# Optimization experiments

Measured on AMD Instinct MI355X. Metric: run time of the kernel, lower is better.

The kernel has to match this reference:

```python
import jax, jax.numpy as jnp
import numpy as np
from jax import lax

T = 512
CHUNK = 64
H = W = 28
C = 4
D_MODEL = H * W * C  # 3136
D_HIDDEN = 512
ALPHA = 0.9
ETA0 = 0.1
P = 2.0
EPS = 1e-6


def setup_inputs() -> dict:
    key = jax.random.key(0)
    ks = jax.random.split(key, 8)
    x = jax.random.normal(ks[0], (T, C, H, W), dtype=jnp.float32)
    conv_k_w = jax.random.normal(ks[1], (3, 3, C, C), dtype=jnp.float32) / 6.0  # lecun-ish: fan_in=36
    conv_v_w = jax.random.normal(ks[2], (3, 3, C, C), dtype=jnp.float32) / 6.0
    conv_k_b = jnp.zeros((C,), jnp.float32)
    conv_v_b = jnp.zeros((C,), jnp.float32)
    rms_k_scale = jnp.ones((C,), jnp.float32)
    rms_v_scale = jnp.ones((C,), jnp.float32)
    W1 = jax.random.normal(ks[3], (D_MODEL, D_HIDDEN), dtype=jnp.float32) / np.sqrt(D_MODEL).astype(np.float32)
    b1 = jnp.zeros((D_HIDDEN,), jnp.float32)
    W2 = jax.random.normal(ks[4], (D_HIDDEN, D_MODEL), dtype=jnp.float32) / np.sqrt(D_HIDDEN).astype(np.float32)
    b2 = jnp.zeros((D_MODEL,), jnp.float32)
    return {"x": x, "conv_k_w": conv_k_w, "conv_k_b": conv_k_b,
            "conv_v_w": conv_v_w, "conv_v_b": conv_v_b,
            "rms_k_scale": rms_k_scale, "rms_v_scale": rms_v_scale,
            "W1": W1, "b1": b1, "W2": W2, "b2": b2}


def _conv(x_nhwc, w, b):
    y = lax.conv_general_dilated(x_nhwc, w, window_strides=(1, 1), padding='SAME',
                                 dimension_numbers=('NHWC', 'HWIO', 'NHWC'))
    return y + b


def _rmsnorm(z, scale):
    inv = lax.rsqrt(jnp.mean(z * z, axis=-1, keepdims=True) + EPS)
    return z * inv * scale


def _mlp(params, k):
    w1, bb1, w2, bb2 = params
    return jax.nn.gelu(k @ w1 + bb1) @ w2 + bb2


def reference(x, conv_k_w, conv_k_b, conv_v_w, conv_v_b, rms_k_scale, rms_v_scale, W1, b1, W2, b2):
    t = x.shape[0]
    xh = jnp.transpose(x, (0, 2, 3, 1))  # [T,H,W,C]
    nk = _rmsnorm(_conv(xh, conv_k_w, conv_k_b), rms_k_scale).reshape(t, -1)  # [T, D_MODEL]
    nv = _rmsnorm(_conv(xh, conv_v_w, conv_v_b), rms_v_scale).reshape(t, -1)

    params0 = (W1, b1, W2, b2)

    def loss_per_token(params, k, v):
        pred = _mlp(params, k)
        return jnp.sum(jnp.abs(pred - v) ** P)

    etas = ETA0 * ALPHA ** jnp.arange(CHUNK, dtype=jnp.float32)
    betas = ALPHA ** jnp.arange(CHUNK, dtype=jnp.float32)
    weights = etas * (betas[-1] / betas)  # [CHUNK]

    n_chunks = t // CHUNK
    Kc = nk.reshape(n_chunks, CHUNK, D_MODEL)
    Vc = nv.reshape(n_chunks, CHUNK, D_MODEL)

    def chunk_body(params, kv):
        K, V = kv
        # per-token parameter grads: leaves have leading CHUNK axis
        grads = jax.vmap(jax.grad(loss_per_token), in_axes=(None, 0, 0))(params, K, V)
        new_params = jax.tree.map(
            lambda p, g: p - jnp.tensordot(weights, g, axes=((0,), (0,))), params, grads)
        Y = _mlp(new_params, K)  # recall on keys with updated fast weights
        return new_params, Y

    _, Y_chunks = lax.scan(chunk_body, params0, (Kc, Vc))
    Y = Y_chunks.reshape(t, D_MODEL)
    return Y.reshape(t, C, H, W)
```

## Files before the change

### kernel.cpp

```cpp
#include <hip/hip_runtime.h>
#include <math.h>

#define DM 3136
#define DH 512

typedef __attribute__((ext_vector_type(8))) short bf16x8;
typedef __attribute__((ext_vector_type(4))) float f32x4;

__device__ __forceinline__ ushort f2bf(float f) {
  union { float f; unsigned u; } v; v.f = f;
  unsigned r = v.u + 0x7FFFu + ((v.u >> 16) & 1u);
  return (ushort)(r >> 16);
}
__device__ __forceinline__ float bf2f(ushort u) {
  union { float f; unsigned u; } v; v.u = ((unsigned)u) << 16;
  return v.f;
}

#define MICRO_4x4 \
    acc[0][0] += a.x*b.x; acc[0][1] += a.x*b.y; acc[0][2] += a.x*b.z; acc[0][3] += a.x*b.w; \
    acc[1][0] += a.y*b.x; acc[1][1] += a.y*b.y; acc[1][2] += a.y*b.z; acc[1][3] += a.y*b.w; \
    acc[2][0] += a.z*b.x; acc[2][1] += a.z*b.y; acc[2][2] += a.z*b.z; acc[2][3] += a.z*b.w; \
    acc[3][0] += a.w*b.x; acc[3][1] += a.w*b.y; acc[3][2] += a.w*b.z; acc[3][3] += a.w*b.w;

__device__ __forceinline__ void gelu_both(float xx, float& g, float& gp) {
  const float c = 0.7978845608028654f;
  const float a = 0.044715f;
  float x2 = xx * xx;
  float u = c * (xx + a * xx * x2);
  float t = tanhf(u);
  g  = 0.5f * xx * (1.f + t);
  gp = 0.5f * (1.f + t) + 0.5f * xx * (1.f - t * t) * c * (1.f + 3.f * a * x2);
}
__device__ __forceinline__ float gelu_only(float xx) {
  const float c = 0.7978845608028654f;
  const float a = 0.044715f;
  float u = c * (xx + a * xx * xx * xx);
  return 0.5f * xx * (1.f + tanhf(u));
}

__device__ __forceinline__ void nt64_core(
    const ushort* __restrict__ A, int lda,
    const ushort* __restrict__ B, int ldb,
    int ksteps, f32x4* acc) {
  int lane = threadIdx.x & 63;
  int wv = threadIdx.x >> 6;
  int qr = wv >> 1, qc = wv & 1;
  int lr = lane & 15;
  int lk = (lane >> 4) << 3;
  const ushort* pa0 = A + (size_t)(qr * 32 + lr) * lda + lk;
  const ushort* pa1 = pa0 + (size_t)16 * lda;
  const ushort* pb0 = B + (size_t)(qc * 32 + lr) * ldb + lk;
  const ushort* pb1 = pb0 + (size_t)16 * ldb;
  bf16x8 a0 = *(const bf16x8*)pa0;
  bf16x8 a1 = *(const bf16x8*)pa1;
  bf16x8 b0 = *(const bf16x8*)pb0;
  bf16x8 b1 = *(const bf16x8*)pb1;
  for (int s = 0; s < ksteps; ++s) {
    int sn = (s + 1 < ksteps) ? (s + 1) * 32 : s * 32;
    bf16x8 na0 = *(const bf16x8*)(pa0 + sn);
    bf16x8 na1 = *(const bf16x8*)(pa1 + sn);
    bf16x8 nb0 = *(const bf16x8*)(pb0 + sn);
    bf16x8 nb1 = *(const bf16x8*)(pb1 + sn);
    acc[0] = __builtin_amdgcn_mfma_f32_16x16x32_bf16(a0, b0, acc[0], 0, 0, 0);
    acc[1] = __builtin_amdgcn_mfma_f32_16x16x32_bf16(a0, b1, acc[1], 0, 0, 0);
    acc[2] = __builtin_amdgcn_mfma_f32_16x16x32_bf16(a1, b0, acc[2], 0, 0, 0);
    acc[3] = __builtin_amdgcn_mfma_f32_16x16x32_bf16(a1, b1, acc[3], 0, 0, 0);
    a0 = na0; a1 = na1; b0 = nb0; b1 = nb1;
  }
}

__device__ __forceinline__ void nt64_store(const f32x4* acc, float* __restrict__ dst, int ldc) {
  int lane = threadIdx.x & 63, wv = threadIdx.x >> 6;
  int r0 = (wv >> 1) * 32 + ((lane >> 4) << 2);
  int c0 = (wv & 1) * 32 + (lane & 15);
  #pragma unroll
  for (int r = 0; r < 4; ++r) {
    dst[(size_t)(r0 + r) * ldc + c0]           = acc[0][r];
    dst[(size_t)(r0 + r) * ldc + c0 + 16]      = acc[1][r];
    dst[(size_t)(r0 + r + 16) * ldc + c0]      = acc[2][r];
    dst[(size_t)(r0 + r + 16) * ldc + c0 + 16] = acc[3][r];
  }
}

__device__ __forceinline__ void dw_epilogue256(
    const f32x4* acc, int n0, const float* __restrict__ Vn,
    const float* __restrict__ b2in, float wc2,
    ushort* __restrict__ Dwb_o, ushort* __restrict__ Dwt_o,
    float* __restrict__ b2out, float* smem) {
  int lane = threadIdx.x & 63, wvv = threadIdx.x >> 6;
  int qr = wvv >> 1, qc = wvv & 1;
  int r0 = qr * 32 + ((lane >> 4) << 2);
  int c0 = qc * 32 + (lane & 15);
  float csum[2] = {0.f, 0.f};
  #pragma unroll
  for (int r = 0; r < 4; ++r) {
    #pragma unroll
    for (int p = 0; p < 4; ++p) {
      int m = r0 + r + ((p >> 1) ? 16 : 0);
      int dl = c0 + ((p & 1) ? 16 : 0);
      int d = n0 + dl;
      float dw = wc2 * (acc[p][r] + b2in[d] - Vn[(size_t)m * DM + d]);
      ushort db = f2bf(dw);
      Dwb_o[(size_t)m * DM + d] = db;
      Dwt_o[(size_t)d * 64 + m] = db;
      csum[p & 1] += dw;
    }
  }
  int slot = qr * 4 + ((lane >> 4) & 3);
  smem[(size_t)c0 * 8 + slot] = csum[0];
  smem[(size_t)(c0 + 16) * 8 + slot] = csum[1];
  __syncthreads();
  if (threadIdx.x < 64) {
    float s = 0.f;
    #pragma unroll
    for (int q = 0; q < 8; ++q) s += smem[threadIdx.x * 8 + q];
    b2out[n0 + threadIdx.x] = b2in[n0 + threadIdx.x] - s;
  }
}

__global__ __launch_bounds__(256) void conv_rms(
    const float* __restrict__ x,
    const float* __restrict__ wk, const float* __restrict__ bk,
    const float* __restrict__ wv, const float* __restrict__ bv,
    const float* __restrict__ sk, const float* __restrict__ sv,
    const float* __restrict__ W1, ushort* __restrict__ w1tb,
    const float* __restrict__ W2, ushort* __restrict__ W2b0, ushort* __restrict__ W2tb0,
    ushort* __restrict__ nkb, float* __restrict__ nv) {
  __shared__ float smem[4160];
  int tid = threadIdx.x;
  if (blockIdx.x >= 1960) {
    int t = blockIdx.x - 1960;
    int d0 = (t % 49) * 64, h0 = (t / 49) * 64;
    int c = tid & 63, rq = tid >> 6;
    #pragma unroll
    for (int q = 0; q < 16; ++q) {
      int r = q * 4 + rq;
      float v = W2[(size_t)(h0 + r) * DM + d0 + c];
      smem[r * 65 + c] = v;
      W2b0[(size_t)(h0 + r) * DM + d0 + c] = f2bf(v);
    }
    __syncthreads();
    #pragma unroll
    for (int q = 0; q < 16; ++q) {
      int r = q * 4 + rq;
      W2tb0[(size_t)(d0 + r) * DH + h0 + c] = f2bf(smem[c * 65 + r]);
    }
    return;
  }
  if (blockIdx.x >= 1568) {
    int t = blockIdx.x - 1568;
    int d0 = (t % 49) * 64, h0 = (t / 49) * 64;
    int c = tid & 63, rq = tid >> 6;
    #pragma unroll
    for (int q = 0; q < 16; ++q) {
      int r = q * 4 + rq;
      smem[r * 65 + c] = W1[(size_t)(d0 + r) * 512 + h0 + c];
    }
    __syncthreads();
    #pragma unroll
    for (int q = 0; q < 16; ++q) {
      int r = q * 4 + rq;
      w1tb[(size_t)(h0 + r) * 3136 + d0 + c] = f2bf(smem[c * 65 + r]);
    }
    return;
  }
  float* swk = smem;
  float* swv = smem + 144;
  float* sb  = smem + 288;
  if (tid < 144) { swk[tid] = wk[tid]; swv[tid] = wv[tid]; }
  if (tid < 4) {
    sb[tid] = bk[tid]; sb[4 + tid] = bv[tid];
    sb[8 + tid] = sk[tid]; sb[12 + tid] = sv[tid];
  }
  __syncthreads();
  int idx = blockIdx.x * 256 + tid;
  int t = idx / 784, hw = idx - t * 784;
  int h = hw / 28, w = hw - h * 28;
  float ak[4], av[4];
  #pragma unroll
  for (int c = 0; c < 4; ++c) { ak[c] = sb[c]; av[c] = sb[4 + c]; }
  const float* xt = x + (size_t)t * DM;
  for (int kh = 0; kh < 3; ++kh) {
    int ih = h + kh - 1;
    if (ih < 0 || ih >= 28) continue;
    for (int kw = 0; kw < 3; ++kw) {
      int iw = w + kw - 1;
      if (iw < 0 || iw >= 28) continue;
      int base = (kh * 3 + kw) * 16;
      #pragma unroll
      for (int ci = 0; ci < 4; ++ci) {
        float xv = xt[ci * 784 + ih * 28 + iw];
        #pragma unroll
        for (int co = 0; co < 4; ++co) {
          ak[co] += xv * swk[base + ci * 4 + co];
          av[co] += xv * swv[base + ci * 4 + co];
        }
      }
    }
  }
  float mk = (ak[0]*ak[0] + ak[1]*ak[1] + ak[2]*ak[2] + ak[3]*ak[3]) * 0.25f + 1e-6f;
  float mv = (av[0]*av[0] + av[1]*av[1] + av[2]*av[2] + av[3]*av[3]) * 0.25f + 1e-6f;
  float ik = 1.f / sqrtf(mk), iv = 1.f / sqrtf(mv);
  ushort4 ok = { f2bf(ak[0]*ik*sb[8]), f2bf(ak[1]*ik*sb[9]),
                 f2bf(ak[2]*ik*sb[10]), f2bf(ak[3]*ik*sb[11]) };
  float4 ov = { av[0]*iv*sb[12], av[1]*iv*sb[13], av[2]*iv*sb[14], av[3]*iv*sb[15] };
  *(ushort4*)&nkb[(size_t)idx * 4] = ok;
  *(float4*)&nv[(size_t)idx * 4] = ov;
}

__global__ __launch_bounds__(256) void u1_kernel(
    const ushort* __restrict__ nkb, const ushort* __restrict__ w1tb,
    float* __restrict__ KKsl, float* __restrict__ Hb_sl) {
  f32x4 acc[4] = {{0.f,0.f,0.f,0.f},{0.f,0.f,0.f,0.f},{0.f,0.f,0.f,0.f},{0.f,0.f,0.f,0.f}};
  int job = blockIdx.x;
  if (job < 448) {
    int s = job % 7;
    int t = job / 7;
    int m0 = (t >> 3) * 64, n0 = (t & 7) * 64;
    nt64_core(nkb + (size_t)m0 * DM + s * 448, DM, w1tb + (size_t)n0 * DM + s * 448, DM, 14, acc);
    nt64_store(acc, Hb_sl + (size_t)s * 262144 + (size_t)m0 * 512 + n0, 512);
  } else {
    int j2 = job - 448;
    int p = j2 / 7, s = j2 % 7;
    int c = 0;
    while ((c + 1) * (c + 2) / 2 <= p) ++c;
    int j = p - c * (c + 1) / 2;
    nt64_core(nkb + (size_t)c * 64 * DM + s * 448, DM, nkb + (size_t)j * 64 * DM + s * 448, DM, 14, acc);
    nt64_store(acc, KKsl + ((size_t)p * 7 + s) * 4096, 64);
  }
}

__global__ __launch_bounds__(256) void u2_kernel(
    const float* __restrict__ KKsl, const float* __restrict__ Hb_sl,
    float* __restrict__ KKf, float* __restrict__ Hbase,
    const float* __restrict__ b1,
    float* __restrict__ Hh, ushort* __restrict__ Gb, ushort* __restrict__ Gtb,
    float* __restrict__ Gp) {
  int i = blockIdx.x * 256 + threadIdx.x;
  if (i < 147456) {
    int pair = i >> 12, e = i & 4095;
    float s = 0.f;
    #pragma unroll
    for (int t = 0; t < 7; ++t) s += KKsl[((size_t)pair * 7 + t) * 4096 + e];
    KKf[i] = s;
  } else {
    int j = i - 147456;
    float s = 0.f;
    #pragma unroll
    for (int t = 0; t < 7; ++t) s += Hb_sl[(size_t)t * 262144 + j];
    Hbase[j] = s;
    if (j < 32768) {
      Hh[j] = s;
      float g, gp;
      gelu_both(s + b1[j & 511], g, gp);
      Gb[j] = f2bf(g);
      Gtb[(j & 511) * 64 + (j >> 9)] = f2bf(g);
      Gp[j] = gp;
    }
  }
}

__device__ __forceinline__ void hs_corr_job(
    const float* __restrict__ KK, const float* __restrict__ Ewj,
    float* __restrict__ dst, int bx, float* smem) {
  float* As = smem;
  float* Bs = smem + 4096;
  int tid = threadIdx.x;
  int n0 = bx * 64;
  {
    int m = tid >> 2, ib = (tid & 3) * 16;
    #pragma unroll
    for (int q = 0; q < 4; ++q) {
      float4 v = *(const float4*)(KK + m * 64 + ib + q * 4);
      As[(ib + q*4 + 0)*64 + m] = v.x;
      As[(ib + q*4 + 1)*64 + m] = v.y;
      As[(ib + q*4 + 2)*64 + m] = v.z;
      As[(ib + q*4 + 3)*64 + m] = v.w;
    }
    int kr = tid >> 4, nn = (tid & 15) * 4;
    #pragma unroll
    for (int q = 0; q < 4; ++q)
      *(float4*)&Bs[(kr + q*16)*64 + nn] = *(const float4*)(Ewj + (size_t)(kr + q*16) * DH + n0 + nn);
  }
  __syncthreads();
  int tx = tid & 15, ty = tid >> 4;
  float acc[4][4] = {{0.f}};
  #pragma unroll 16
  for (int kk = 0; kk < 64; ++kk) {
    float4 a = *(const float4*)&As[kk*64 + ty * 4];
    float4 b = *(const float4*)&Bs[kk*64 + tx * 4];
    MICRO_4x4
  }
  #pragma unroll
  for (int r = 0; r < 4; ++r) {
    float4 v = { acc[r][0], acc[r][1], acc[r][2], acc[r][3] };
    *(float4*)&dst[(ty*4 + r) * DH + n0 + tx*4] = v;
  }
}

__global__ __launch_bounds__(256) void pred0_kernel(
    const ushort* __restrict__ Gb0, const ushort* __restrict__ W2tb0,
    const float* __restrict__ V, const float* __restrict__ b2in, float wc2,
    float* __restrict__ b2out, ushort* __restrict__ Dwb_o, ushort* __restrict__ Dwt_o) {
  __shared__ float smem[512];
  f32x4 acc[4] = {{0.f,0.f,0.f,0.f},{0.f,0.f,0.f,0.f},{0.f,0.f,0.f,0.f},{0.f,0.f,0.f,0.f}};
  int n0 = blockIdx.x * 64;
  nt64_core(Gb0, 512, W2tb0 + (size_t)n0 * 512, 512, 16, acc);
  dw_epilogue256(acc, n0, V, b2in, wc2, Dwb_o, Dwt_o, b2out, smem);
}

__global__ __launch_bounds__(256) void p4w2_kernel(
    const ushort* __restrict__ Dwb, const ushort* __restrict__ Dwtb,
    const ushort* __restrict__ Gtb, const ushort* __restrict__ W2b_c,
    ushort* __restrict__ W2b_n, ushort* __restrict__ W2tb_n,
    float* __restrict__ Esl) {
  f32x4 acc[4] = {{0.f,0.f,0.f,0.f},{0.f,0.f,0.f,0.f},{0.f,0.f,0.f,0.f},{0.f,0.f,0.f,0.f}};
  int b = blockIdx.x;
  if (b < 56) {
    int s = b % 7, nt = b / 7;
    nt64_core(Dwb + s * 448, DM, W2b_c + (size_t)nt * 64 * DM + s * 448, DM, 14, acc);
    nt64_store(acc, Esl + (size_t)s * 32768 + nt * 64, 512);
  } else {
    int li = b - 56;
    int d0 = (li % 49) * 64, h0 = (li / 49) * 64;
    nt64_core(Gtb + (size_t)h0 * 64, 64, Dwtb + (size_t)d0 * 64, 64, 2, acc);
    int lane = threadIdx.x & 63, wvv = threadIdx.x >> 6;
    int r0 = (wvv >> 1) * 32 + ((lane >> 4) << 2);
    int c0 = (wvv & 1) * 32 + (lane & 15);
    #pragma unroll
    for (int r = 0; r < 4; ++r) {
      #pragma unroll
      for (int p = 0; p < 4; ++p) {
        int h = h0 + r0 + r + ((p >> 1) ? 16 : 0);
        int d = d0 + c0 + ((p & 1) ? 16 : 0);
        size_t off = (size_t)h * DM + d;
        float w = bf2f(W2b_c[off]) - acc[p][r];
        ushort wb = f2bf(w);
        W2b_n[off] = wb;
        W2tb_n[(size_t)d * DH + h] = wb;
      }
    }
  }
}

__global__ __launch_bounds__(256) void g2hr_kernel(
    const float* __restrict__ KKf, int ch,
    const float* __restrict__ Esl, const float* __restrict__ GpC,
    const float* __restrict__ Hcur, const float* __restrict__ b1e,
    float* __restrict__ b1o, ushort* __restrict__ G2b, float* __restrict__ EwOut,
    const float* __restrict__ Hcorr, const float* __restrict__ Hbase_n,
    float* __restrict__ HhN, ushort* __restrict__ GbN,
    ushort* __restrict__ GtbN, float* __restrict__ GpN) {
  __shared__ float smem[5200];
  int blk = blockIdx.x;
  int tid = threadIdx.x;
  int tri = ch * (ch + 1) / 2;
  if (blk < 32) {
    float* KKs = smem;
    float* Ews = smem + 4160;
    float* b1l = smem + 5184;
    const float* KKcc = KKf + (size_t)(tri + ch) * 4096;
    int n0 = blk * 16;
    #pragma unroll
    for (int q = 0; q < 16; ++q) {
      int e = q * 256 + tid;
      KKs[(e >> 6) * 65 + (e & 63)] = KKcc[e];
    }
    #pragma unroll
    for (int q = 0; q < 4; ++q) {
      int e = q * 256 + tid;
      int i = e >> 4, cc = e & 15;
      size_t off = (size_t)i * 512 + n0 + cc;
      float s = 0.f;
      #pragma unroll
      for (int sl = 0; sl < 7; ++sl) s += Esl[(size_t)sl * 32768 + off];
      Ews[e] = s * GpC[off];
    }
    __syncthreads();
    if (tid < 16) {
      float s = 0.f;
      for (int i = 0; i < 64; ++i) s += Ews[i * 16 + tid];
      b1l[tid] = b1e[n0 + tid] - s;
    }
    __syncthreads();
    #pragma unroll
    for (int q = 0; q < 4; ++q) {
      int e = q * 256 + tid;
      int mrow = e >> 4, cc = e & 15;
      float corr = 0.f;
      #pragma unroll 16
      for (int i = 0; i < 64; ++i) corr += KKs[mrow * 65 + i] * Ews[i * 16 + cc];
      float xx = Hcur[(size_t)mrow * 512 + n0 + cc] - corr + b1l[cc];
      G2b[(size_t)mrow * 512 + n0 + cc] = f2bf(gelu_only(xx));
    }
  } else if (blk < 40) {
    float* Bs = smem;
    int bx = blk - 32;
    int n0 = bx * 64;
    #pragma unroll
    for (int q = 0; q < 16; ++q) {
      int e = q * 256 + tid;
      int k = e >> 6, c = e & 63;
      size_t off = (size_t)k * 512 + n0 + c;
      float s = 0.f;
      #pragma unroll
      for (int sl = 0; sl < 7; ++sl) s += Esl[(size_t)sl * 32768 + off];
      float ew = s * GpC[off];
      Bs[k * 64 + c] = ew;
      EwOut[off] = ew;
    }
    __syncthreads();
    if (tid < 64) {
      float s = 0.f;
      for (int k = 0; k < 64; ++k) s += Bs[k * 64 + tid];
      b1o[n0 + tid] = b1e[n0 + tid] - s;
    }
  } else {
    float* Ewt = smem;
    float* KKs = smem + 1024;
    float* b1l = smem + 2064;
    int bh = blk - 40;
    int m0 = (bh >> 5) * 16;
    int c0 = (bh & 31) * 16;
    #pragma unroll
    for (int q = 0; q < 4; ++q) {
      int e = q * 256 + tid;
      int i = e >> 4, cl = e & 15;
      size_t off = (size_t)i * 512 + c0 + cl;
      float s = 0.f;
      #pragma unroll
      for (int sl = 0; sl < 7; ++sl) s += Esl[(size_t)sl * 32768 + off];
      Ewt[i * 16 + cl] = s * GpC[off];
    }
    const float* KK = KKf + (size_t)((ch + 1) * (ch + 2) / 2 + ch) * 4096;
    #pragma unroll
    for (int q = 0; q < 4; ++q) {
      int e = q * 256 + tid;
      int ml = e >> 6, i = e & 63;
      KKs[ml * 65 + i] = KK[(m0 + ml) * 64 + i];
    }
    __syncthreads();
    if (tid < 16) {
      float s = 0.f;
      for (int i = 0; i < 64; ++i) s += Ewt[i * 16 + tid];
      b1l[tid] = b1e[c0 + tid] - s;
    }
    __syncthreads();
    int ml = tid >> 4, cl = tid & 15;
    int m = m0 + ml, c = c0 + cl;
    float corr = 0.f;
    #pragma unroll 16
    for (int i = 0; i < 64; ++i) corr += KKs[ml * 65 + i] * Ewt[i * 16 + cl];
    size_t off = (size_t)m * 512 + c;
    float s = Hbase_n[off] - corr;
    for (int j = 0; j < ch; ++j) s -= Hcorr[(size_t)j * 32768 + off];
    HhN[off] = s;
    float g, gp;
    gelu_both(s + b1l[cl], g, gp);
    GbN[off] = f2bf(g);
    GtbN[(size_t)c * 64 + m] = f2bf(g);
    GpN[off] = gp;
  }
}

__global__ __launch_bounds__(256) void yp3_kernel(
    const ushort* __restrict__ G2b, const ushort* __restrict__ W2tb,
    const float* __restrict__ b2n, float* __restrict__ out, int t0,
    const ushort* __restrict__ Gnb, const float* __restrict__ Vn, float wc2,
    float* __restrict__ b2out, ushort* __restrict__ Dwb, ushort* __restrict__ Dwtb,
    const float* __restrict__ KKf, int ch,
    const float* __restrict__ Ewst, float* __restrict__ Hcorr) {
  __shared__ float smem[8192];
  int b = blockIdx.x;
  if (b < 49) {
    f32x4 acc[4] = {{0.f,0.f,0.f,0.f},{0.f,0.f,0.f,0.f},{0.f,0.f,0.f,0.f},{0.f,0.f,0.f,0.f}};
    int n0 = b * 64;
    nt64_core(G2b, 512, W2tb + (size_t)n0 * 512, 512, 16, acc);
    int lane = threadIdx.x & 63, wvv = threadIdx.x >> 6;
    int r0 = (wvv >> 1) * 32 + ((lane >> 4) << 2);
    int c0 = (wvv & 1) * 32 + (lane & 15);
    #pragma unroll
    for (int r = 0; r < 4; ++r) {
      #pragma unroll
      for (int p = 0; p < 4; ++p) {
        int m = r0 + r + ((p >> 1) ? 16 : 0);
        int d = n0 + c0 + ((p & 1) ? 16 : 0);
        out[(size_t)(t0 + m) * DM + d] = acc[p][r] + b2n[d];
      }
    }
  } else if (ch < 7 && b < 98) {
    f32x4 acc[4] = {{0.f,0.f,0.f,0.f},{0.f,0.f,0.f,0.f},{0.f,0.f,0.f,0.f},{0.f,0.f,0.f,0.f}};
    int n0 = (b - 49) * 64;
    nt64_core(Gnb, 512, W2tb + (size_t)n0 * 512, 512, 16, acc);
    dw_epilogue256(acc, n0, Vn, b2n, wc2, Dwb, Dwtb, b2out, smem);
  } else {
    int j2 = b - (ch < 7 ? 98 : 49);
    int j = j2 >> 3, bx = j2 & 7;
    int trin = (ch + 2) * (ch + 3) / 2;
    hs_corr_job(KKf + (size_t)(trin + j) * 4096, Ewst + (size_t)j * 32768,
                Hcorr + (size_t)j * 32768, bx, smem);
  }
}

extern "C" void kernel_launch(void* const* d_in, const int* in_sizes, int n_in,
                              void* d_out, int out_size, void* d_ws, size_t ws_size,
                              hipStream_t stream) {
  const float* x  = (const float*)d_in[0];
  const float* wk = (const float*)d_in[1];
  const float* bk = (const float*)d_in[2];
  const float* wv = (const float*)d_in[3];
  const float* bv = (const float*)d_in[4];
  const float* sk = (const float*)d_in[5];
  const float* sv = (const float*)d_in[6];
  const float* W1 = (const float*)d_in[7];
  const float* b1 = (const float*)d_in[8];
  const float* W2 = (const float*)d_in[9];
  const float* b2 = (const float*)d_in[10];
  float* out = (float*)d_out;
  float* ws  = (float*)d_ws;

  ushort* nkb   = (ushort*)ws;
  ushort* w1tb  = (ushort*)(ws + 802816);
  float* nv     = ws + 1605632;
  float* bf_base = nv + 1605632;
  ushort* W2b0  = (ushort*)bf_base;
  ushort* W2tb0 = (ushort*)(bf_base + 802816);
  ushort* W2bA  = (ushort*)(bf_base + 1605632);
  ushort* W2bB  = (ushort*)(bf_base + 2408448);
  ushort* W2tbA = (ushort*)(bf_base + 3211264);
  ushort* W2tbB = (ushort*)(bf_base + 4014080);
  float* Esl    = bf_base + 4816896;
  float* Hb_sl  = Esl + 229376;
  float* KKsl   = Hb_sl + 1835008;
  float* Hbase  = KKsl + 1032192;
  float* KKf    = Hbase + 262144;
  float* HhA    = KKf + 147456;
  float* HhB    = HhA + 32768;
  float* GpA    = HhB + 32768;
  float* GpB    = GpA + 32768;
  ushort* GbA   = (ushort*)(GpB + 32768);
  ushort* GbB   = (ushort*)(GpB + 49152);
  ushort* GtbA  = (ushort*)(GpB + 65536);
  ushort* GtbB  = (ushort*)(GpB + 81920);
  ushort* G2b   = (ushort*)(GpB + 98304);
  ushort* Dwb   = (ushort*)(GpB + 114688);
  ushort* Dwtb  = (ushort*)(GpB + 215040);
  float* Ewst   = GpB + 315392;
  float* Hcorr  = Ewst + 262144;
  float* b1A    = Hcorr + 229376;
  float* b1B    = b1A + 512;
  float* b2A    = b1B + 512;
  float* b2B    = b2A + 3136;

  ushort* W2bb[2]   = { W2bA, W2bB };
  ushort* W2tbb[2]  = { W2tbA, W2tbB };
  ushort* Gbb[2]    = { GbA, GbB };
  ushort* Gtbb[2]   = { GtbA, GtbB };
  float* Hhb[2]     = { HhA, HhB };
  float* Gpb[2]     = { GpA, GpB };
  float* b1buf[2]   = { b1A, b1B };
  float* b2buf[2]   = { b2A, b2B };

  float wc2 = 2.0f * (float)(0.1 * pow(0.9, 63.0));

  conv_rms<<<2352, 256, 0, stream>>>(x, wk, bk, wv, bv, sk, sv,
                                     W1, w1tb, W2, W2b0, W2tb0, nkb, nv);
  u1_kernel<<<700, 256, 0, stream>>>(nkb, w1tb, KKsl, Hb_sl);
  u2_kernel<<<1600, 256, 0, stream>>>(KKsl, Hb_sl, KKf, Hbase, b1, HhA, GbA, GtbA, GpA);
  pred0_kernel<<<49, 256, 0, stream>>>(GbA, W2tb0, nv, b2, wc2, b2A, Dwb, Dwtb);

  for (int ch = 0; ch < 8; ++ch) {
    const float* b1e  = ch ? b1buf[(ch - 1) & 1] : b1;
    const ushort* W2b_c = ch ? W2bb[(ch - 1) & 1] : W2b0;

    p4w2_kernel<<<448, 256, 0, stream>>>(
        Dwb, Dwtb, Gtbb[ch & 1], W2b_c,
        W2bb[ch & 1], W2tbb[ch & 1], Esl);
    g2hr_kernel<<<(ch < 7 ? 168 : 32), 256, 0, stream>>>(
        KKf, ch, Esl, Gpb[ch & 1], Hhb[ch & 1], b1e, b1buf[ch & 1],
        G2b, Ewst + (size_t)ch * 32768,
        Hcorr, Hbase + (size_t)((ch + 1) & 7) * 32768,
        Hhb[(ch + 1) & 1], Gbb[(ch + 1) & 1], Gtbb[(ch + 1) & 1], Gpb[(ch + 1) & 1]);
    int g3 = 49 + (ch < 7 ? 49 : 0) + (ch < 6 ? 8 * (ch + 1) : 0);
    yp3_kernel<<<g3, 256, 0, stream>>>(
        G2b, W2tbb[ch & 1], b2buf[ch & 1], out, ch * 64,
        Gbb[(ch + 1) & 1], nv + (size_t)((ch + 1) & 7) * 200704, wc2,
        b2buf[(ch + 1) & 1], Dwb, Dwtb,
        KKf, ch, Ewst, Hcorr);
  }
}
```

Measured before the change: 351.1 us.

## Fuse E-slice GEMM and G2/H-recompute stages into a single kernel

Merges the p4w2 and g2hr kernels into one launch. The W2 update blocks stay the same. The 56 split-K blocks that wrote 7 partial E slices are replaced by 32 blocks, each computing a full-K 64x16 E tile with a dedicated MFMA loop and consuming it in registers and LDS. This removes the Esl round-trip through global memory, one kernel launch per chunk, and the 7-way partial-sum reads. In exchange, each of those 32 blocks now runs a long 98-step serial K loop with no split-K parallelism, and handles both the G2 and next-chunk H recompute, which may put them on the critical path.

```diff
diff --git a/kernel.cpp b/kernel.cpp
--- a/kernel.cpp
+++ b/kernel.cpp
@@ -310,22 +310,25 @@
   dw_epilogue256(acc, n0, V, b2in, wc2, Dwb_o, Dwt_o, b2out, smem);
 }
 
-__global__ __launch_bounds__(256) void p4w2_kernel(
+__global__ __launch_bounds__(256) void ab_kernel(
     const ushort* __restrict__ Dwb, const ushort* __restrict__ Dwtb,
     const ushort* __restrict__ Gtb, const ushort* __restrict__ W2b_c,
     ushort* __restrict__ W2b_n, ushort* __restrict__ W2tb_n,
-    float* __restrict__ Esl) {
-  f32x4 acc[4] = {{0.f,0.f,0.f,0.f},{0.f,0.f,0.f,0.f},{0.f,0.f,0.f,0.f},{0.f,0.f,0.f,0.f}};
+    const float* __restrict__ KKf, int ch,
+    const float* __restrict__ GpC, const float* __restrict__ Hcur,
+    const float* __restrict__ b1e, float* __restrict__ b1o,
+    ushort* __restrict__ G2b, float* __restrict__ EwOut,
+    const float* __restrict__ Hcorr, const float* __restrict__ Hbase_n,
+    float* __restrict__ HhN, ushort* __restrict__ GbN,
+    ushort* __restrict__ GtbN, float* __restrict__ GpN) {
+  __shared__ float smem[9360];
   int b = blockIdx.x;
-  if (b < 56) {
-    int s = b % 7, nt = b / 7;
-    nt64_core(Dwb + s * 448, DM, W2b_c + (size_t)nt * 64 * DM + s * 448, DM, 14, acc);
-    nt64_store(acc, Esl + (size_t)s * 32768 + nt * 64, 512);
-  } else {
-    int li = b - 56;
-    int d0 = (li % 49) * 64, h0 = (li / 49) * 64;
+  int tid = threadIdx.x;
+  if (b < 392) {
+    f32x4 acc[4] = {{0.f,0.f,0.f,0.f},{0.f,0.f,0.f,0.f},{0.f,0.f,0.f,0.f},{0.f,0.f,0.f,0.f}};
+    int d0 = (b % 49) * 64, h0 = (b / 49) * 64;
     nt64_core(Gtb + (size_t)h0 * 64, 64, Dwtb + (size_t)d0 * 64, 64, 2, acc);
-    int lane = threadIdx.x & 63, wvv = threadIdx.x >> 6;
+    int lane = tid & 63, wvv = tid >> 6;
     int r0 = (wvv >> 1) * 32 + ((lane >> 4) << 2);
     int c0 = (wvv & 1) * 32 + (lane & 15);
     #pragma unroll
@@ -341,126 +344,99 @@
         W2tb_n[(size_t)d * DH + h] = wb;
       }
     }
-  }
-}
-
-__global__ __launch_bounds__(256) void g2hr_kernel(
-    const float* __restrict__ KKf, int ch,
-    const float* __restrict__ Esl, const float* __restrict__ GpC,
-    const float* __restrict__ Hcur, const float* __restrict__ b1e,
-    float* __restrict__ b1o, ushort* __restrict__ G2b, float* __restrict__ EwOut,
-    const float* __restrict__ Hcorr, const float* __restrict__ Hbase_n,
-    float* __restrict__ HhN, ushort* __restrict__ GbN,
-    ushort* __restrict__ GtbN, float* __restrict__ GpN) {
-  __shared__ float smem[5200];
-  int blk = blockIdx.x;
-  int tid = threadIdx.x;
-  int tri = ch * (ch + 1) / 2;
-  if (blk < 32) {
-    float* KKs = smem;
-    float* Ews = smem + 4160;
-    float* b1l = smem + 5184;
-    const float* KKcc = KKf + (size_t)(tri + ch) * 4096;
-    int n0 = blk * 16;
-    #pragma unroll
-    for (int q = 0; q < 16; ++q) {
-      int e = q * 256 + tid;
-      KKs[(e >> 6) * 65 + (e & 63)] = KKcc[e];
-    }
-    #pragma unroll
-    for (int q = 0; q < 4; ++q) {
-      int e = q * 256 + tid;
-      int i = e >> 4, cc = e & 15;
-      size_t off = (size_t)i * 512 + n0 + cc;
-      float s = 0.f;
-      #pragma unroll
-      for (int sl = 0; sl < 7; ++sl) s += Esl[(size_t)sl * 32768 + off];
-      Ews[e] = s * GpC[off];
+  } else {
+    float* KK1 = smem;
+    float* KK2 = smem + 4160;
+    float* sEw = smem + 8320;
+    float* b1l = smem + 9344;
+    int sb = b - 392;
+    int n0 = sb * 16;
+    int tri = ch * (ch + 1) / 2;
+    int lane = tid & 63, w = tid >> 6;
+    int lr = lane & 15, lk = (lane >> 4) << 3;
+    const ushort* pa = Dwb + (size_t)(w * 16 + lr) * DM + lk;
+    const ushort* pb = W2b_c + (size_t)(n0 + lr) * DM + lk;
+    f32x4 acc = {0.f, 0.f, 0.f, 0.f};
+    bf16x8 a = *(const bf16x8*)pa;
+    bf16x8 bb = *(const bf16x8*)pb;
+    for (int s = 0; s < 98; ++s) {
+      int sn = (s + 1 < 98) ? (s + 1) * 32 : s * 32;
+      bf16x8 na = *(const bf16x8*)(pa + sn);
+      bf16x8 nb = *(const bf16x8*)(pb + sn);
+      acc = __builtin_amdgcn_mfma_f32_16x16x32_bf16(a, bb, acc, 0, 0, 0);
+      a = na; bb = nb;
+    }
+    {
+      const float* KKcc = KKf + (size_t)(tri + ch) * 4096;
+      #pragma unroll
+      for (int q = 0; q < 16; ++q) {
+        int e = q * 256 + tid;
+        KK1[(e >> 6) * 65 + (e & 63)] = KKcc[e];
+      }
+      if (ch < 7) {
+        const float* KKn = KKf + (size_t)((ch + 1) * (ch + 2) / 2 + ch) * 4096;
+        #pragma unroll
+        for (int q = 0; q < 16; ++q) {
+          int e = q * 256 + tid;
+          KK2[(e >> 6) * 65 + (e & 63)] = KKn[e];
+        }
+      }
+    }
+    {
+      int row0 = w * 16 + ((lane >> 4) << 2);
+      int col = lane & 15;
+      #pragma unroll
+      for (int r = 0; r < 4; ++r) {
+        int k = row0 + r;
+        sEw[k * 16 + col] = acc[r] * GpC[(size_t)k * 512 + n0 + col];
+      }
     }
     __syncthreads();
     if (tid < 16) {
       float s = 0.f;
-      for (int i = 0; i < 64; ++i) s += Ews[i * 16 + tid];
-      b1l[tid] = b1e[n0 + tid] - s;
+      for (int i = 0; i < 64; ++i) s += sEw[i * 16 + tid];
+      float nb1 = b1e[n0 + tid] - s;
+      b1l[tid] = nb1;
+      if (ch < 7) b1o[n0 + tid] = nb1;
+    }
+    if (ch < 6) {
+      #pragma unroll
+      for (int q = 0; q < 4; ++q) {
+        int e = q * 256 + tid;
+        int k = e >> 4, cl = e & 15;
+        EwOut[(size_t)k * 512 + n0 + cl] = sEw[e];
+      }
     }
     __syncthreads();
     #pragma unroll
     for (int q = 0; q < 4; ++q) {
       int e = q * 256 + tid;
-      int mrow = e >> 4, cc = e & 15;
+      int m = e >> 4, cl = e & 15;
       float corr = 0.f;
       #pragma unroll 16
-      for (int i = 0; i < 64; ++i) corr += KKs[mrow * 65 + i] * Ews[i * 16 + cc];
-      float xx = Hcur[(size_t)mrow * 512 + n0 + cc] - corr + b1l[cc];
-      G2b[(size_t)mrow * 512 + n0 + cc] = f2bf(gelu_only(xx));
-    }
-  } else if (blk < 40) {
-    float* Bs = smem;
-    int bx = blk - 32;
-    int n0 = bx * 64;
-    #pragma unroll
-    for (int q = 0; q < 16; ++q) {
-      int e = q * 256 + tid;
-      int k = e >> 6, c = e & 63;
-      size_t off = (size_t)k * 512 + n0 + c;
-      float s = 0.f;
-      #pragma unroll
-      for (int sl = 0; sl < 7; ++sl) s += Esl[(size_t)sl * 32768 + off];
-      float ew = s * GpC[off];
-      Bs[k * 64 + c] = ew;
-      EwOut[off] = ew;
-    }
-    __syncthreads();
-    if (tid < 64) {
-      float s = 0.f;
-      for (int k = 0; k < 64; ++k) s += Bs[k * 64 + tid];
-      b1o[n0 + tid] = b1e[n0 + tid] - s;
-    }
-  } else {
-    float* Ewt = smem;
-    float* KKs = smem + 1024;
-    float* b1l = smem + 2064;
-    int bh = blk - 40;
-    int m0 = (bh >> 5) * 16;
-    int c0 = (bh & 31) * 16;
-    #pragma unroll
-    for (int q = 0; q < 4; ++q) {
-      int e = q * 256 + tid;
-      int i = e >> 4, cl = e & 15;
-      size_t off = (size_t)i * 512 + c0 + cl;
-      float s = 0.f;
-      #pragma unroll
-      for (int sl = 0; sl < 7; ++sl) s += Esl[(size_t)sl * 32768 + off];
-      Ewt[i * 16 + cl] = s * GpC[off];
-    }
-    const float* KK = KKf + (size_t)((ch + 1) * (ch + 2) / 2 + ch) * 4096;
-    #pragma unroll
-    for (int q = 0; q < 4; ++q) {
-      int e = q * 256 + tid;
-      int ml = e >> 6, i = e & 63;
-      KKs[ml * 65 + i] = KK[(m0 + ml) * 64 + i];
-    }
-    __syncthreads();
-    if (tid < 16) {
-      float s = 0.f;
-      for (int i = 0; i < 64; ++i) s += Ewt[i * 16 + tid];
-      b1l[tid] = b1e[c0 + tid] - s;
-    }
-    __syncthreads();
-    int ml = tid >> 4, cl = tid & 15;
-    int m = m0 + ml, c = c0 + cl;
-    float corr = 0.f;
-    #pragma unroll 16
-    for (int i = 0; i < 64; ++i) corr += KKs[ml * 65 + i] * Ewt[i * 16 + cl];
-    size_t off = (size_t)m * 512 + c;
-    float s = Hbase_n[off] - corr;
-    for (int j = 0; j < ch; ++j) s -= Hcorr[(size_t)j * 32768 + off];
-    HhN[off] = s;
-    float g, gp;
-    gelu_both(s + b1l[cl], g, gp);
-    GbN[off] = f2bf(g);
-    GtbN[(size_t)c * 64 + m] = f2bf(g);
-    GpN[off] = gp;
+      for (int i = 0; i < 64; ++i) corr += KK1[m * 65 + i] * sEw[i * 16 + cl];
+      float xx = Hcur[(size_t)m * 512 + n0 + cl] - corr + b1l[cl];
+      G2b[(size_t)m * 512 + n0 + cl] = f2bf(gelu_only(xx));
+    }
+    if (ch < 7) {
+      #pragma unroll
+      for (int q = 0; q < 4; ++q) {
+        int e = q * 256 + tid;
+        int m = e >> 4, cl = e & 15;
+        float corrH = 0.f;
+        #pragma unroll 16
+        for (int i = 0; i < 64; ++i) corrH += KK2[m * 65 + i] * sEw[i * 16 + cl];
+        size_t off = (size_t)m * 512 + n0 + cl;
+        float s = Hbase_n[off] - corrH;
+        for (int j = 0; j < ch; ++j) s -= Hcorr[(size_t)j * 32768 + off];
+        HhN[off] = s;
+        float g, gp;
+        gelu_both(s + b1l[cl], g, gp);
+        GbN[off] = f2bf(g);
+        GtbN[(size_t)(n0 + cl) * 64 + m] = f2bf(g);
+        GpN[off] = gp;
+      }
+    }
   }
 }
 
@@ -574,11 +550,10 @@
     const float* b1e  = ch ? b1buf[(ch - 1) & 1] : b1;
     const ushort* W2b_c = ch ? W2bb[(ch - 1) & 1] : W2b0;
 
-    p4w2_kernel<<<448, 256, 0, stream>>>(
+    ab_kernel<<<424, 256, 0, stream>>>(
         Dwb, Dwtb, Gtbb[ch & 1], W2b_c,
-        W2bb[ch & 1], W2tbb[ch & 1], Esl);
-    g2hr_kernel<<<(ch < 7 ? 168 : 32), 256, 0, stream>>>(
-        KKf, ch, Esl, Gpb[ch & 1], Hhb[ch & 1], b1e, b1buf[ch & 1],
+        W2bb[ch & 1], W2tbb[ch & 1],
+        KKf, ch, Gpb[ch & 1], Hhb[ch & 1], b1e, b1buf[ch & 1],
         G2b, Ewst + (size_t)ch * 32768,
         Hcorr, Hbase + (size_t)((ch + 1) & 7) * 32768,
         Hhb[(ch + 1) & 1], Gbb[(ch + 1) & 1], Gtbb[(ch + 1) & 1], Gpb[(ch + 1) & 1]);
```

Measured after the change: 554.7 us. +58.0%, slower.
